# Kernel tuning notes

Hardware: AMD Instinct MI355X
Metric: run time of the kernel (lower is better)

The kernel has to match this reference:

```python
import jax, jax.numpy as jnp
import numpy as np

B = 64        # batch_size (graphs)
N_HITS = 1024 # nodes per graph
D = 64        # input_dim == output_dim (hidden)
E = 16 * B * N_HITS // 16 * 16  # 1,048,576 edges (16 per node avg)


def setup_inputs() -> dict:
    key = jax.random.key(0)
    ks = jax.random.split(key, 12)
    x = jax.random.normal(ks[0], (B * N_HITS, D), dtype=jnp.float32)
    # edges constrained within each graph (PyG-style batched edge_index)
    g = jax.random.randint(ks[1], (E,), 0, B)
    s_loc = jax.random.randint(ks[2], (E,), 0, N_HITS)
    e_loc = jax.random.randint(ks[3], (E,), 0, N_HITS)
    edge_index = jnp.stack([g * N_HITS + s_loc, g * N_HITS + e_loc], axis=0).astype(jnp.int64)
    batch = jnp.repeat(jnp.arange(B, dtype=jnp.int64), N_HITS)  # node -> graph id
    s = 0.05
    return {
        "x": x,
        "edge_index": edge_index,
        "batch": batch,
        "batch_size": B,
        "weight": jax.random.normal(ks[4], (D, D), dtype=jnp.float32) * s,
        "bias": jax.random.normal(ks[5], (D,), dtype=jnp.float32) * s,
        "w1": jax.random.normal(ks[6], (D, D), dtype=jnp.float32) * s,
        "b1": jax.random.normal(ks[7], (D,), dtype=jnp.float32) * s,
        "w2": jax.random.normal(ks[8], (D, D), dtype=jnp.float32) * s,
        "b2": jax.random.normal(ks[9], (D,), dtype=jnp.float32) * s,
        "w3": jax.random.normal(ks[10], (D, 1), dtype=jnp.float32) * s,
        "b3": jax.random.normal(ks[11], (1,), dtype=jnp.float32) * s,
    }


def reference(x, edge_index, batch, batch_size, weight, bias, w1, b1, w2, b2, w3, b3):
    n_hits = x.shape[0] // batch_size
    nodes = x.reshape(batch_size, n_hits, x.shape[1])  # [B, n, d]
    start, end = edge_index[0], edge_index[1]
    g = batch[start]
    # dense adjacency scatter: A[g, start_local, end_local] = 1.0 (is_e=False branch)
    A = jnp.zeros((batch_size, n_hits, n_hits), dtype=x.dtype)
    A = A.at[g, start - n_hits * g, end - n_hits * g].set(1.0)
    # GraphConv: y = (A @ x) @ W + bias
    y = jnp.einsum('bij,bjd->bid', A, nodes)
    y = y @ weight + bias  # [B, n, d]
    # agg='max': torch.max(nodes, dim=1)[0] -> values
    pooled = jnp.max(y, axis=1)  # [B, d]
    # MLP: Linear-Tanh-Linear-Tanh-Linear
    h = jnp.tanh(pooled @ w1 + b1)
    h = jnp.tanh(h @ w2 + b2)
    return h @ w3 + b3  # [B, 1] logits
```

## Files before the change

kernel.cpp:

```cpp
#include <hip/hip_runtime.h>
#include <hip/hip_bf16.h>


#define NNODES 65536
#define NGRAPH 64
#define NLOCAL 1024
#define DIM 64
#define MASK_WORDS 32
#define KMAX 64
#define CHUNK_ROWS 128
#define NBIN 256
#define NBUCKET 512
#define SEGCAP 32

__device__ __forceinline__ unsigned f2ord(float f) {
    unsigned u = __float_as_uint(f);
    return (u & 0x80000000u) ? ~u : (u | 0x80000000u);
}
__device__ __forceinline__ float ord2f(unsigned u) {
    return (u & 0x80000000u) ? __uint_as_float(u & 0x7FFFFFFFu)
                             : __uint_as_float(~u);
}

__global__ __launch_bounds__(256) void clear_kernel(uint4* __restrict__ p, int n4)
{
    int i = blockIdx.x * 256 + threadIdx.x;
    int stride = gridDim.x * 256;
    uint4 z = {0u, 0u, 0u, 0u};
    for (; i < n4; i += stride) p[i] = z;
}

__global__ __launch_bounds__(256) void bin_kernel(
    const int* __restrict__ ei, int E,
    unsigned* __restrict__ seg, unsigned short* __restrict__ segcnt,
    unsigned* __restrict__ pooled_u)
{
    __shared__ unsigned off[NBUCKET];
    int tid = threadIdx.x;
    off[tid] = 0u;
    off[tid + 256] = 0u;
    if (blockIdx.x < 16) pooled_u[blockIdx.x * 256 + tid] = 0u;
    __syncthreads();
    int perblk = (E + NBIN - 1) / NBIN;
    int e0 = blockIdx.x * perblk;
    int e1 = min(e0 + perblk, E);
    unsigned* myseg = seg + (size_t)blockIdx.x * NBUCKET * SEGCAP;
    for (int e = e0 + tid; e < e1; e += 256) {
        int s = ei[e];
        int t = ei[E + e] & (NLOCAL - 1);
        int sl = s & (NLOCAL - 1);
        int bk = ((s >> 10) << 3) | (sl >> 7);
        unsigned slot = atomicAdd(&off[bk], 1u);
        if (slot < SEGCAP) myseg[bk * SEGCAP + slot] = (unsigned)((sl << 10) | t);
    }
    __syncthreads();
    unsigned c0 = off[tid], c1 = off[tid + 256];
    segcnt[blockIdx.x * NBUCKET + tid]       = (unsigned short)(c0 < SEGCAP ? c0 : SEGCAP);
    segcnt[blockIdx.x * NBUCKET + tid + 256] = (unsigned short)(c1 < SEGCAP ? c1 : SEGCAP);
}

__global__ __launch_bounds__(256) void xw_kernel(
    const float* __restrict__ x, const float* __restrict__ W,
    float* __restrict__ xw)
{
    __shared__ float4 xlds[64 * 16];
    int tid = threadIdx.x;
    int row0 = blockIdx.x * 64;
    const float4* xg4 = (const float4*)(x + (size_t)row0 * DIM);
    for (int i = tid; i < 64 * 16; i += 256) xlds[i] = xg4[i];
    int col = tid & 63;
    int rg  = tid >> 6;
    float w[64];
    #pragma unroll
    for (int k = 0; k < 64; ++k) w[k] = W[k * DIM + col];
    __syncthreads();
    #pragma unroll
    for (int rr = 0; rr < 16; ++rr) {
        int row = rg * 16 + rr;
        float acc = 0.f;
        #pragma unroll
        for (int k4 = 0; k4 < 16; ++k4) {
            float4 xv = xlds[row * 16 + k4];
            acc = fmaf(xv.x, w[4 * k4 + 0], acc);
            acc = fmaf(xv.y, w[4 * k4 + 1], acc);
            acc = fmaf(xv.z, w[4 * k4 + 2], acc);
            acc = fmaf(xv.w, w[4 * k4 + 3], acc);
        }
        xw[(size_t)(row0 + row) * DIM + col] = acc;
    }
}

__global__ __launch_bounds__(1024) void agg_fused_kernel(
    const float* __restrict__ xw, const float* __restrict__ bias,
    const unsigned* __restrict__ seg, const unsigned short* __restrict__ segcnt,
    unsigned* __restrict__ pooled_u)
{
    __shared__ unsigned mask[CHUNK_ROWS * MASK_WORDS];
    __shared__ float red[16 * DIM];

    int tid = threadIdx.x;
    int lane = tid & 63, wave = tid >> 6;
    int b = blockIdx.x;
    int g = ((b >> 6) << 3) | (b & 7);
    int chunk = (b >> 3) & 7;
    int bk = (g << 3) | chunk;

    for (int i = tid; i < CHUNK_ROWS * MASK_WORDS; i += 1024) mask[i] = 0u;
    __syncthreads();

    for (int idx = tid; idx < NBIN * SEGCAP; idx += 1024) {
        int sb = idx >> 5;
        int sl = idx & 31;
        int n = segcnt[sb * NBUCKET + bk];
        if (sl < n) {
            unsigned pk = seg[((size_t)sb * NBUCKET + bk) * SEGCAP + sl];
            int r = (pk >> 10) & (CHUNK_ROWS - 1);
            int t = pk & (NLOCAL - 1);
            atomicOr(&mask[r * MASK_WORDS + (t >> 5)], 1u << (t & 31));
        }
    }
    __syncthreads();

    const float* xwg = xw + ((size_t)g << 10) * DIM;
    float bv = bias[lane];
    float vmax = -INFINITY;
    unsigned short* lists = (unsigned short*)mask;

    for (int i = 0; i < 8; i += 2) {
        int rowa = wave * 8 + i;
        int rowb = rowa + 1;
        int myrow = (lane < 32) ? rowa : rowb;
        unsigned bits = mask[myrow * MASK_WORDS + (lane & 31)];
        int c = __popc(bits);
        int inc = c;
        #pragma unroll
        for (int d = 1; d < 32; d <<= 1) {
            int v = __shfl_up(inc, d, 32);
            if ((lane & 31) >= d) inc += v;
        }
        {
            int off = inc - c;
            unsigned short* lr = lists + myrow * KMAX;
            while (bits) {
                int bb = __ffs(bits) - 1;
                bits &= bits - 1;
                if (off < KMAX) lr[off] = (unsigned short)((lane & 31) * 32 + bb);
                ++off;
            }
        }
        int cca = __shfl(inc, 31, 64);
        int ccb = __shfl(inc, 63, 64);
        cca = cca < KMAX ? cca : KMAX;
        ccb = ccb < KMAX ? ccb : KMAX;
        #pragma unroll
        for (int half = 0; half < 2; ++half) {
            int row = half ? rowb : rowa;
            int cc = half ? ccb : cca;
            const unsigned* lr32 = (const unsigned*)(lists + row * KMAX);
            float a0 = 0.f, a1 = 0.f, a2 = 0.f, a3 = 0.f;
            float a4 = 0.f, a5 = 0.f, a6 = 0.f, a7 = 0.f;
            int j = 0;
            for (; j + 8 <= cc; j += 8) {
                unsigned p0 = lr32[(j >> 1) + 0], p1 = lr32[(j >> 1) + 1];
                unsigned p2 = lr32[(j >> 1) + 2], p3 = lr32[(j >> 1) + 3];
                a0 += xwg[(p0 & 0xFFFF) * DIM + lane];
                a1 += xwg[(p0 >> 16) * DIM + lane];
                a2 += xwg[(p1 & 0xFFFF) * DIM + lane];
                a3 += xwg[(p1 >> 16) * DIM + lane];
                a4 += xwg[(p2 & 0xFFFF) * DIM + lane];
                a5 += xwg[(p2 >> 16) * DIM + lane];
                a6 += xwg[(p3 & 0xFFFF) * DIM + lane];
                a7 += xwg[(p3 >> 16) * DIM + lane];
            }
            for (; j + 2 <= cc; j += 2) {
                unsigned p0 = lr32[j >> 1];
                a0 += xwg[(p0 & 0xFFFF) * DIM + lane];
                a1 += xwg[(p0 >> 16) * DIM + lane];
            }
            if (j < cc) {
                unsigned p0 = lr32[j >> 1];
                a0 += xwg[(p0 & 0xFFFF) * DIM + lane];
            }
            float s = ((a0 + a1) + (a2 + a3)) + ((a4 + a5) + (a6 + a7)) + bv;
            vmax = fmaxf(vmax, s);
        }
    }

    red[wave * DIM + lane] = vmax;
    __syncthreads();
    if (wave == 0) {
        float m = red[lane];
        #pragma unroll
        for (int w = 1; w < 16; ++w) m = fmaxf(m, red[w * DIM + lane]);
        atomicMax(&pooled_u[g * DIM + lane], f2ord(m));
    }
}

__global__ __launch_bounds__(64) void mlp_kernel(
    const unsigned* __restrict__ pooled_u,
    const float* __restrict__ w1, const float* __restrict__ b1,
    const float* __restrict__ w2, const float* __restrict__ b2,
    const float* __restrict__ w3, const float* __restrict__ b3,
    float* __restrict__ out)
{
    __shared__ float buf[DIM];
    __shared__ float buf2[DIM];
    int g = blockIdx.x, l = threadIdx.x;
    buf[l] = ord2f(pooled_u[g * DIM + l]);
    __syncthreads();
    float h = b1[l];
    for (int k = 0; k < DIM; ++k) h = fmaf(buf[k], w1[k * DIM + l], h);
    buf2[l] = tanhf(h);
    __syncthreads();
    float h2 = b2[l];
    for (int k = 0; k < DIM; ++k) h2 = fmaf(buf2[k], w2[k * DIM + l], h2);
    h2 = tanhf(h2);
    float v = h2 * w3[l];
    #pragma unroll
    for (int off = 32; off; off >>= 1) v += __shfl_down(v, off, 64);
    if (l == 0) out[g] = v + b3[0];
}

__global__ __launch_bounds__(256) void scatter_kernel(
    const int* __restrict__ ei, unsigned* __restrict__ mask, int E)
{
    int e = blockIdx.x * 256 + threadIdx.x;
    if (e >= E) return;
    int start = ei[e];
    int col   = ei[E + e] & (NLOCAL - 1);
    atomicOr(&mask[(size_t)start * MASK_WORDS + (col >> 5)], 1u << (col & 31));
}

__global__ __launch_bounds__(256) void agg_kernel(
    const float* __restrict__ x, const float* __restrict__ weight,
    const float* __restrict__ bias, const unsigned* __restrict__ mask,
    unsigned* __restrict__ pooled_u)
{
    __shared__ float Wlds[DIM * DIM];
    __shared__ float blds[DIM];
    int tid = threadIdx.x;
    for (int i = tid; i < DIM * DIM; i += 256) Wlds[i] = weight[i];
    if (tid < DIM) blds[tid] = bias[tid];
    __syncthreads();
    int lane = tid & 63;
    int wave = tid >> 6;
    int rowbase = blockIdx.x * 64 + wave * 16;
    int g = rowbase >> 10;
    const float* xg = x + ((size_t)g << 10) * DIM;
    float vmax = -INFINITY;
    for (int rr = 0; rr < 16; ++rr) {
        int row = rowbase + rr;
        const unsigned* mrow = mask + (size_t)row * MASK_WORDS;
        float acc = 0.f;
        for (int w = 0; w < MASK_WORDS; ++w) {
            unsigned bits = mrow[w];
            while (bits) {
                int b = __ffs(bits) - 1;
                bits &= bits - 1;
                acc += xg[(size_t)(w * 32 + b) * DIM + lane];
            }
        }
        float y = blds[lane];
        for (int k = 0; k < DIM; ++k) {
            float a = __shfl(acc, k, 64);
            y = fmaf(a, Wlds[k * DIM + lane], y);
        }
        vmax = fmaxf(vmax, y);
    }
    atomicMax(&pooled_u[g * DIM + lane], f2ord(vmax));
}

__global__ __launch_bounds__(1024) void fused_kernel(
    const float* __restrict__ x, const int* __restrict__ ei, int E,
    const float* __restrict__ weight, const float* __restrict__ bias,
    const float* __restrict__ w1, const float* __restrict__ b1,
    const float* __restrict__ w2, const float* __restrict__ b2,
    const float* __restrict__ w3, const float* __restrict__ b3,
    float* __restrict__ out)
{
    __shared__ unsigned mask[256 * MASK_WORDS];
    __shared__ float Wlds[DIM * DIM];
    __shared__ float blds[DIM];
    __shared__ float red[16 * DIM];
    __shared__ float pool[DIM];
    __shared__ float hbuf[DIM];
    int tid = threadIdx.x;
    int g = blockIdx.x;
    int lane = tid & 63;
    int wave = tid >> 6;
    const float* xg = x + ((size_t)g << 10) * DIM;
    for (int i = tid; i < DIM * DIM; i += 1024) Wlds[i] = weight[i];
    if (tid < DIM) blds[tid] = bias[tid];
    float vmax = -INFINITY;
    for (int chunk = 0; chunk < NLOCAL / 256; ++chunk) {
        int row0 = chunk * 256;
        __syncthreads();
        for (int i = tid; i < 256 * MASK_WORDS; i += 1024) mask[i] = 0u;
        __syncthreads();
        int lo = (g << 10) + row0, hi = lo + 256;
        for (int e = tid; e < E; e += 1024) {
            int s = ei[e];
            if (s >= lo && s < hi) {
                int t = ei[E + e] & (NLOCAL - 1);
                atomicOr(&mask[(s - lo) * MASK_WORDS + (t >> 5)], 1u << (t & 31));
            }
        }
        __syncthreads();
        for (int rr = 0; rr < 256 / 16; ++rr) {
            int row = wave * (256 / 16) + rr;
            float acc = 0.f;
            for (int w = 0; w < MASK_WORDS; ++w) {
                unsigned bits = mask[row * MASK_WORDS + w];
                while (bits) {
                    int b = __ffs(bits) - 1;
                    bits &= bits - 1;
                    acc += xg[(size_t)(w * 32 + b) * DIM + lane];
                }
            }
            float y = blds[lane];
            for (int k = 0; k < DIM; ++k) {
                float a = __shfl(acc, k, 64);
                y = fmaf(a, Wlds[k * DIM + lane], y);
            }
            vmax = fmaxf(vmax, y);
        }
    }
    red[wave * DIM + lane] = vmax;
    __syncthreads();
    if (tid < DIM) {
        float m = red[tid];
        #pragma unroll
        for (int w = 1; w < 16; ++w) m = fmaxf(m, red[w * DIM + tid]);
        pool[tid] = m;
    }
    __syncthreads();
    if (tid < DIM) {
        float h = b1[tid];
        for (int k = 0; k < DIM; ++k) h = fmaf(pool[k], w1[k * DIM + tid], h);
        hbuf[tid] = tanhf(h);
    }
    __syncthreads();
    if (tid < DIM) {
        float h2 = b2[tid];
        for (int k = 0; k < DIM; ++k) h2 = fmaf(hbuf[k], w2[k * DIM + tid], h2);
        h2 = tanhf(h2);
        red[tid] = h2 * w3[tid];
    }
    __syncthreads();
    if (tid == 0) {
        float v = b3[0];
        for (int k = 0; k < DIM; ++k) v += red[k];
        out[g] = v;
    }
}

extern "C" void kernel_launch(void* const* d_in, const int* in_sizes, int n_in,
                              void* d_out, int out_size, void* d_ws, size_t ws_size,
                              hipStream_t stream)
{
    const float* x      = (const float*)d_in[0];
    const int*   ei     = (const int*)d_in[1];
    const float* weight = (const float*)d_in[4];
    const float* bias   = (const float*)d_in[5];
    const float* w1     = (const float*)d_in[6];
    const float* b1     = (const float*)d_in[7];
    const float* w2     = (const float*)d_in[8];
    const float* b2     = (const float*)d_in[9];
    const float* w3     = (const float*)d_in[10];
    const float* b3     = (const float*)d_in[11];
    float* out = (float*)d_out;

    const int E = in_sizes[1] / 2;

    const size_t PL_BYTES  = (size_t)NGRAPH * DIM * 4;
    const size_t SC_BYTES  = (size_t)NBIN * NBUCKET * 2;
    const size_t SEG_BYTES = (size_t)NBIN * NBUCKET * SEGCAP * 4;
    const size_t XW_BYTES  = (size_t)NNODES * DIM * 4;
    const size_t need_A = PL_BYTES + SC_BYTES + SEG_BYTES + XW_BYTES;
    const size_t MASKW  = (size_t)NNODES * MASK_WORDS;
    const size_t need_B = MASKW * 4 + PL_BYTES;

    if (d_ws != nullptr && ws_size >= need_A) {
        char* base = (char*)d_ws;
        unsigned*       pooled_u = (unsigned*)base;
        unsigned short* segcnt   = (unsigned short*)(base + PL_BYTES);
        unsigned*       seg      = (unsigned*)(base + PL_BYTES + SC_BYTES);
        float*          xw       = (float*)(base + PL_BYTES + SC_BYTES + SEG_BYTES);

        bin_kernel<<<NBIN, 256, 0, stream>>>(ei, E, seg, segcnt, pooled_u);
        xw_kernel<<<NNODES / 64, 256, 0, stream>>>(x, weight, xw);
        agg_fused_kernel<<<NBUCKET, 1024, 0, stream>>>(xw, bias, seg, segcnt, pooled_u);
        mlp_kernel<<<NGRAPH, DIM, 0, stream>>>(pooled_u, w1, b1, w2, b2, w3, b3, out);
    } else if (d_ws != nullptr && ws_size >= need_B) {
        unsigned* mask     = (unsigned*)d_ws;
        unsigned* pooled_u = mask + MASKW;
        clear_kernel<<<1024, 256, 0, stream>>>((uint4*)mask, (int)((MASKW * 4 + PL_BYTES) / 16));
        scatter_kernel<<<(E + 255) / 256, 256, 0, stream>>>(ei, mask, E);
        agg_kernel<<<NNODES / 64, 256, 0, stream>>>(x, weight, bias, mask, pooled_u);
        mlp_kernel<<<NGRAPH, DIM, 0, stream>>>(pooled_u, w1, b1, w2, b2, w3, b3, out);
    } else {
        fused_kernel<<<NGRAPH, 1024, 0, stream>>>(
            x, ei, E, weight, bias, w1, b1, w2, b2, w3, b3, out);
    }
}
```

Before: 71.80 us.

## Tile xw rows through LDS in aggregation and fuse MLP via last-block

The aggregation kernel now streams each graph's 1024 transformed rows through shared memory in 128-row tiles. Each row walks its sorted neighbor list against the current tile, replacing scattered global gathers with LDS reads. The separate MLP launch is removed: the last block to finish, detected with an atomic counter, computes the MLP for all graphs. The xw kernel's block-to-row mapping is also remapped so a graph's rows land on the same XCD as the aggregation blocks that read them. In exchange, every block now loads a whole graph's xw (8x redundant traffic across chunks), and adds per-tile syncs and a serial tail in one block.

```diff
diff --git a/kernel.cpp b/kernel.cpp
--- a/kernel.cpp
+++ b/kernel.cpp
@@ -9,6 +9,8 @@
 #define MASK_WORDS 32
 #define KMAX 64
 #define CHUNK_ROWS 128
+#define TILE_ROWS 128
+#define NTILE 8
 #define NBIN 256
 #define NBUCKET 512
 #define SEGCAP 32
@@ -33,13 +35,14 @@
 __global__ __launch_bounds__(256) void bin_kernel(
     const int* __restrict__ ei, int E,
     unsigned* __restrict__ seg, unsigned short* __restrict__ segcnt,
-    unsigned* __restrict__ pooled_u)
+    unsigned* __restrict__ pooled_u, unsigned* __restrict__ done)
 {
     __shared__ unsigned off[NBUCKET];
     int tid = threadIdx.x;
     off[tid] = 0u;
     off[tid + 256] = 0u;
     if (blockIdx.x < 16) pooled_u[blockIdx.x * 256 + tid] = 0u;
+    if (blockIdx.x == 16 && tid == 0) *done = 0u;
     __syncthreads();
     int perblk = (E + NBIN - 1) / NBIN;
     int e0 = blockIdx.x * perblk;
@@ -65,7 +68,12 @@
 {
     __shared__ float4 xlds[64 * 16];
     int tid = threadIdx.x;
-    int row0 = blockIdx.x * 64;
+    int b = blockIdx.x;
+    int xcd = b & 7, idx = b >> 3;
+    int g = ((idx >> 4) << 3) | xcd;
+    int sub = idx & 15;
+    int row0 = (g << 10) + (sub << 6);
+
     const float4* xg4 = (const float4*)(x + (size_t)row0 * DIM);
     for (int i = tid; i < 64 * 16; i += 256) xlds[i] = xg4[i];
     int col = tid & 63;
@@ -90,13 +98,19 @@
     }
 }
 
-__global__ __launch_bounds__(1024) void agg_fused_kernel(
+__global__ __launch_bounds__(1024) void agg_tiled_kernel(
     const float* __restrict__ xw, const float* __restrict__ bias,
     const unsigned* __restrict__ seg, const unsigned short* __restrict__ segcnt,
-    unsigned* __restrict__ pooled_u)
+    unsigned* __restrict__ pooled_u, unsigned* __restrict__ done,
+    const float* __restrict__ w1, const float* __restrict__ b1,
+    const float* __restrict__ w2, const float* __restrict__ b2,
+    const float* __restrict__ w3, const float* __restrict__ b3,
+    float* __restrict__ out)
 {
     __shared__ unsigned mask[CHUNK_ROWS * MASK_WORDS];
+    __shared__ float tile[TILE_ROWS * DIM];
     __shared__ float red[16 * DIM];
+    __shared__ unsigned lastflag;
 
     int tid = threadIdx.x;
     int lane = tid & 63, wave = tid >> 6;
@@ -108,9 +122,9 @@
     for (int i = tid; i < CHUNK_ROWS * MASK_WORDS; i += 1024) mask[i] = 0u;
     __syncthreads();
 
-    for (int idx = tid; idx < NBIN * SEGCAP; idx += 1024) {
-        int sb = idx >> 5;
-        int sl = idx & 31;
+    for (int idx0 = tid; idx0 < NBIN * SEGCAP; idx0 += 1024) {
+        int sb = idx0 >> 5;
+        int sl = idx0 & 31;
         int n = segcnt[sb * NBUCKET + bk];
         if (sl < n) {
             unsigned pk = seg[((size_t)sb * NBUCKET + bk) * SEGCAP + sl];
@@ -121,15 +135,12 @@
     }
     __syncthreads();
 
-    const float* xwg = xw + ((size_t)g << 10) * DIM;
-    float bv = bias[lane];
-    float vmax = -INFINITY;
     unsigned short* lists = (unsigned short*)mask;
-
+    int cc[8];
+    #pragma unroll
     for (int i = 0; i < 8; i += 2) {
         int rowa = wave * 8 + i;
-        int rowb = rowa + 1;
-        int myrow = (lane < 32) ? rowa : rowb;
+        int myrow = rowa + ((lane >> 5) & 1);
         unsigned bits = mask[myrow * MASK_WORDS + (lane & 31)];
         int c = __popc(bits);
         int inc = c;
@@ -138,53 +149,56 @@
             int v = __shfl_up(inc, d, 32);
             if ((lane & 31) >= d) inc += v;
         }
-        {
-            int off = inc - c;
-            unsigned short* lr = lists + myrow * KMAX;
-            while (bits) {
-                int bb = __ffs(bits) - 1;
-                bits &= bits - 1;
-                if (off < KMAX) lr[off] = (unsigned short)((lane & 31) * 32 + bb);
-                ++off;
-            }
+        int off = inc - c;
+        unsigned short* lr = lists + myrow * KMAX;
+        while (bits) {
+            int bb = __ffs(bits) - 1;
+            bits &= bits - 1;
+            if (off < KMAX) lr[off] = (unsigned short)((lane & 31) * 32 + bb);
+            ++off;
         }
         int cca = __shfl(inc, 31, 64);
         int ccb = __shfl(inc, 63, 64);
-        cca = cca < KMAX ? cca : KMAX;
-        ccb = ccb < KMAX ? ccb : KMAX;
+        cc[i]     = cca < KMAX ? cca : KMAX;
+        cc[i + 1] = ccb < KMAX ? ccb : KMAX;
+    }
+
+    const float* xwg = xw + ((size_t)g << 10) * DIM;
+    float acc[8];
+    int idx[8];
+    #pragma unroll
+    for (int i = 0; i < 8; ++i) { acc[i] = 0.f; idx[i] = 0; }
+
+    for (int k = 0; k < NTILE; ++k) {
+        __syncthreads();
+        const float4* src = (const float4*)(xwg + (size_t)k * TILE_ROWS * DIM);
+        float4* dst = (float4*)tile;
+        dst[tid] = src[tid];
+        dst[tid + 1024] = src[tid + 1024];
+        __syncthreads();
+        int hi = (k + 1) * TILE_ROWS;
+        int base = k * TILE_ROWS;
         #pragma unroll
-        for (int half = 0; half < 2; ++half) {
-            int row = half ? rowb : rowa;
-            int cc = half ? ccb : cca;
-            const unsigned* lr32 = (const unsigned*)(lists + row * KMAX);
-            float a0 = 0.f, a1 = 0.f, a2 = 0.f, a3 = 0.f;
-            float a4 = 0.f, a5 = 0.f, a6 = 0.f, a7 = 0.f;
-            int j = 0;
-            for (; j + 8 <= cc; j += 8) {
-                unsigned p0 = lr32[(j >> 1) + 0], p1 = lr32[(j >> 1) + 1];
-                unsigned p2 = lr32[(j >> 1) + 2], p3 = lr32[(j >> 1) + 3];
-                a0 += xwg[(p0 & 0xFFFF) * DIM + lane];
-                a1 += xwg[(p0 >> 16) * DIM + lane];
-                a2 += xwg[(p1 & 0xFFFF) * DIM + lane];
-                a3 += xwg[(p1 >> 16) * DIM + lane];
-                a4 += xwg[(p2 & 0xFFFF) * DIM + lane];
-                a5 += xwg[(p2 >> 16) * DIM + lane];
-                a6 += xwg[(p3 & 0xFFFF) * DIM + lane];
-                a7 += xwg[(p3 >> 16) * DIM + lane];
-            }
-            for (; j + 2 <= cc; j += 2) {
-                unsigned p0 = lr32[j >> 1];
-                a0 += xwg[(p0 & 0xFFFF) * DIM + lane];
-                a1 += xwg[(p0 >> 16) * DIM + lane];
-            }
-            if (j < cc) {
-                unsigned p0 = lr32[j >> 1];
-                a0 += xwg[(p0 & 0xFFFF) * DIM + lane];
-            }
-            float s = ((a0 + a1) + (a2 + a3)) + ((a4 + a5) + (a6 + a7)) + bv;
-            vmax = fmaxf(vmax, s);
-        }
-    }
+        for (int i = 0; i < 8; ++i) {
+            int row = wave * 8 + i;
+            const unsigned short* lr = lists + row * KMAX;
+            int j = idx[i], c = cc[i];
+            float a = acc[i];
+            while (j < c) {
+                int t = lr[j];
+                if (t >= hi) break;
+                a += tile[(t - base) * DIM + lane];
+                ++j;
+            }
+            acc[i] = a;
+            idx[i] = j;
+        }
+    }
+
+    float bv = bias[lane];
+    float vmax = -INFINITY;
+    #pragma unroll
+    for (int i = 0; i < 8; ++i) vmax = fmaxf(vmax, acc[i] + bv);
 
     red[wave * DIM + lane] = vmax;
     __syncthreads();
@@ -193,6 +207,34 @@
         #pragma unroll
         for (int w = 1; w < 16; ++w) m = fmaxf(m, red[w * DIM + lane]);
         atomicMax(&pooled_u[g * DIM + lane], f2ord(m));
+    }
+    if (tid == 0) {
+        __threadfence();
+        unsigned v = atomicAdd(done, 1u);
+        lastflag = (v == NBUCKET - 1) ? 1u : 0u;
+    }
+    __syncthreads();
+    if (lastflag) {
+        for (int gg = 0; gg < 4; ++gg) {
+            int g2 = wave * 4 + gg;
+            float pl = ord2f(atomicOr(&pooled_u[g2 * DIM + lane], 0u));
+            float h = b1[lane];
+            for (int k2 = 0; k2 < 64; ++k2) {
+                float a = __shfl(pl, k2, 64);
+                h = fmaf(a, w1[k2 * DIM + lane], h);
+            }
+            h = tanhf(h);
+            float h2 = b2[lane];
+            for (int k2 = 0; k2 < 64; ++k2) {
+                float a = __shfl(h, k2, 64);
+                h2 = fmaf(a, w2[k2 * DIM + lane], h2);
+            }
+            h2 = tanhf(h2);
+            float v2 = h2 * w3[lane];
+            #pragma unroll
+            for (int o = 32; o; o >>= 1) v2 += __shfl_down(v2, o, 64);
+            if (lane == 0) out[g2] = v2 + b3[0];
+        }
     }
 }
 
@@ -372,7 +414,7 @@
 
     const int E = in_sizes[1] / 2;
 
-    const size_t PL_BYTES  = (size_t)NGRAPH * DIM * 4;
+    const size_t PL_BYTES  = (size_t)NGRAPH * DIM * 4 + 64;
     const size_t SC_BYTES  = (size_t)NBIN * NBUCKET * 2;
     const size_t SEG_BYTES = (size_t)NBIN * NBUCKET * SEGCAP * 4;
     const size_t XW_BYTES  = (size_t)NNODES * DIM * 4;
@@ -383,18 +425,20 @@
     if (d_ws != nullptr && ws_size >= need_A) {
         char* base = (char*)d_ws;
         unsigned*       pooled_u = (unsigned*)base;
+        unsigned*       done     = (unsigned*)(base + (size_t)NGRAPH * DIM * 4);
         unsigned short* segcnt   = (unsigned short*)(base + PL_BYTES);
         unsigned*       seg      = (unsigned*)(base + PL_BYTES + SC_BYTES);
         float*          xw       = (float*)(base + PL_BYTES + SC_BYTES + SEG_BYTES);
 
-        bin_kernel<<<NBIN, 256, 0, stream>>>(ei, E, seg, segcnt, pooled_u);
+        bin_kernel<<<NBIN, 256, 0, stream>>>(ei, E, seg, segcnt, pooled_u, done);
         xw_kernel<<<NNODES / 64, 256, 0, stream>>>(x, weight, xw);
-        agg_fused_kernel<<<NBUCKET, 1024, 0, stream>>>(xw, bias, seg, segcnt, pooled_u);
-        mlp_kernel<<<NGRAPH, DIM, 0, stream>>>(pooled_u, w1, b1, w2, b2, w3, b3, out);
+        agg_tiled_kernel<<<NBUCKET, 1024, 0, stream>>>(
+            xw, bias, seg, segcnt, pooled_u, done,
+            w1, b1, w2, b2, w3, b3, out);
     } else if (d_ws != nullptr && ws_size >= need_B) {
         unsigned* mask     = (unsigned*)d_ws;
         unsigned* pooled_u = mask + MASKW;
-        clear_kernel<<<1024, 256, 0, stream>>>((uint4*)mask, (int)((MASKW * 4 + PL_BYTES) / 16));
+        clear_kernel<<<1024, 256, 0, stream>>>((uint4*)mask, (int)((MASKW * 4 + 16384) / 16));
         scatter_kernel<<<(E + 255) / 256, 256, 0, stream>>>(ei, mask, E);
         agg_kernel<<<NNODES / 64, 256, 0, stream>>>(x, weight, bias, mask, pooled_u);
         mlp_kernel<<<NGRAPH, DIM, 0, stream>>>(pooled_u, w1, b1, w2, b2, w3, b3, out);
```

After: 122.2 us. 70.3% more time.
